# Kernel optimization log

Hardware: AMD Instinct MI355X
Metric: run time of the kernel (lower is better)

## Reference

```python
import jax, jax.numpy as jnp
import numpy as np

ALPHA = 1.702  # sigmoid-GLU scale
LIMIT = 7.0    # clamp limit
TOP_K = 2      # num_experts_per_tok


def setup_inputs() -> dict:
    key = jax.random.key(0)
    ks = jax.random.split(key, 4)
    B, S, H, E, I = 2, 1024, 1024, 8, 2048
    return {
        "hidden_states": jax.random.normal(ks[0], (B, S, H), jnp.float32),
        "router_weight": jax.random.normal(ks[1], (E, H), jnp.float32),
        "router_bias": jnp.zeros((E,), jnp.float32),
        "gate_up_proj": jax.random.normal(ks[2], (E, H, 2 * I), jnp.float32) * 0.02,
        "gate_up_bias": jnp.zeros((E, 2 * I), jnp.float32),
        "down_proj": jax.random.normal(ks[3], (E, I, H), jnp.float32) * 0.02,
        "down_bias": jnp.zeros((E, H), jnp.float32),
    }


def reference(hidden_states, router_weight, router_bias, gate_up_proj,
              gate_up_bias, down_proj, down_bias):
    B, S, H = hidden_states.shape
    E, _, two_I = gate_up_proj.shape
    I = two_I // 2

    flat = hidden_states.reshape(B * S, H)  # [T, H]

    # Router: softmax + top-k
    logits = flat @ router_weight.T + router_bias            # [T, E]
    scores = jax.nn.softmax(logits, axis=-1)
    topk_w, topk_idx = jax.lax.top_k(scores, TOP_K)          # [T, K]

    # Dense per-expert gated FFN (einsum 'abmh,ehn->abemn' computes all experts
    # on all tokens; the reshape/permute dance is a mathematical no-op).
    gu = jnp.einsum('th,ehn->ten', flat, gate_up_proj) + gate_up_bias  # [T, E, 2I]
    gate = jnp.minimum(gu[..., :I], LIMIT)
    up = jnp.clip(gu[..., I:], -LIMIT, LIMIT)
    glu = gate * jax.nn.sigmoid(gate * ALPHA)
    act = (up + 1.0) * glu                                   # [T, E, I]

    down = jnp.einsum('tei,eih->teh', act, down_proj) + down_bias  # [T, E, H]

    # Combine: gather each token's top-k expert outputs, weighted sum.
    gathered = jnp.take_along_axis(down, topk_idx[:, :, None], axis=1)  # [T, K, H]
    out = (gathered * topk_w[:, :, None]).sum(axis=1)        # [T, H]
    return out.reshape(B, S, H)
```

## Files before the change

kernel.cpp:

```cpp
#include <hip/hip_runtime.h>
#include <math.h>

#define TT 2048
#define HH 1024
#define EE 8
#define II 2048
#define N1 4096
#define ALPHA 1.702f
#define LIMIT 7.0f

typedef __attribute__((ext_vector_type(8))) short short8;
typedef __attribute__((ext_vector_type(4))) float floatx4;
typedef __attribute__((ext_vector_type(4))) unsigned int uintx4;

__device__ __forceinline__ short f2bf(float f) {
  union { float f; unsigned u; } v; v.f = f;
  unsigned r = (v.u + 0x7fffu + ((v.u >> 16) & 1u)) >> 16;
  return (short)r;
}
__device__ __forceinline__ unsigned cvt2(float lo, float hi) {
  unsigned r;
  asm("v_cvt_pk_bf16_f32 %0, %1, %2" : "=v"(r) : "v"(lo), "v"(hi));
  return r;
}
__device__ __forceinline__ void gload16(const void* g, void* l) {
  __builtin_amdgcn_global_load_lds(
      (const __attribute__((address_space(1))) unsigned int*)g,
      (__attribute__((address_space(3))) unsigned int*)l, 16, 0, 0);
}

__global__ __launch_bounds__(256) void transpose_all(
    const float* __restrict__ gup, const float* __restrict__ dp,
    unsigned short* __restrict__ gupt, unsigned short* __restrict__ dpt,
    int* __restrict__ counts) {
  const int id = blockIdx.x;
  if (id == 0 && threadIdx.x < 16) counts[threadIdx.x] = 0;
  const float* src;
  unsigned short* dst;
  int K, N, n0, k0, e;
  if (id < 8192) {
    src = gup; dst = gupt; K = HH; N = N1;
    n0 = (id & 63) * 64; k0 = ((id >> 6) & 15) * 64; e = id >> 10;
  } else {
    const int id2 = id - 8192;
    src = dp; dst = dpt; K = II; N = HH;
    n0 = (id2 & 15) * 64; k0 = ((id2 >> 4) & 31) * 64; e = id2 >> 9;
  }
  __shared__ float tile[64][68];
  const float* s = src + (size_t)e * K * N;
  unsigned short* d = dst + (size_t)e * N * K;
  const int t = threadIdx.x;
  const int nq = t & 15, kr = t >> 4;
#pragma unroll
  for (int r = 0; r < 4; r++) {
    const int k = r * 16 + kr;
    const float4 v = *(const float4*)(s + (size_t)(k0 + k) * N + n0 + nq * 4);
    tile[k][nq * 4 + 0] = v.x; tile[k][nq * 4 + 1] = v.y;
    tile[k][nq * 4 + 2] = v.z; tile[k][nq * 4 + 3] = v.w;
  }
  __syncthreads();
  const int n = t >> 2, ks = (t & 3) * 16;
  unsigned short* orow = d + (size_t)(n0 + n) * K + k0 + ks;
  uintx4 w0, w1;
#pragma unroll
  for (int m = 0; m < 4; m++)
    w0[m] = cvt2(tile[ks + 2 * m][n], tile[ks + 2 * m + 1][n]);
#pragma unroll
  for (int m = 0; m < 4; m++)
    w1[m] = cvt2(tile[ks + 8 + 2 * m][n], tile[ks + 9 + 2 * m][n]);
  *(uintx4*)orow = w0;
  *(uintx4*)(orow + 8) = w1;
}

__global__ __launch_bounds__(256) void router_kernel(
    const float* __restrict__ x, const float* __restrict__ rw,
    const float* __restrict__ rb, float* __restrict__ topk_w,
    int* __restrict__ counts, int* __restrict__ rows,
    unsigned short* __restrict__ xb, float* __restrict__ out) {
  const int t = blockIdx.x;
  const float* xr = x + (size_t)t * HH;
  const int lane = threadIdx.x & 63;
  const int wave = threadIdx.x >> 6;
  const float4 z = {0.f, 0.f, 0.f, 0.f};
  ((float4*)(out + (size_t)t * HH))[threadIdx.x] = z;
  float xv[16];
#pragma unroll
  for (int i = 0; i < 16; i++) xv[i] = xr[lane + i * 64];
  __shared__ float logits[EE];
#pragma unroll
  for (int ee = 0; ee < 2; ee++) {
    const int e = wave * 2 + ee;
    const float* wr = rw + (size_t)e * HH;
    float s = 0.f;
#pragma unroll
    for (int i = 0; i < 16; i++) s += xv[i] * wr[lane + i * 64];
#pragma unroll
    for (int off = 32; off > 0; off >>= 1) s += __shfl_down(s, off, 64);
    if (lane == 0) logits[e] = s + rb[e];
  }
  if (wave == 0) {
    unsigned short* xo = xb + (size_t)t * HH;
#pragma unroll
    for (int i = 0; i < 16; i++) xo[lane + i * 64] = (unsigned short)f2bf(xv[i]);
  }
  __syncthreads();
  if (threadIdx.x == 0) {
    float l[EE], sc[EE];
    float mx = -3.4e38f;
    for (int i = 0; i < EE; i++) { l[i] = logits[i]; mx = fmaxf(mx, l[i]); }
    float sum = 0.f;
    for (int i = 0; i < EE; i++) { sc[i] = expf(l[i] - mx); sum += sc[i]; }
    const float inv = 1.f / sum;
    int i0 = 0;
    for (int i = 1; i < EE; i++) if (sc[i] > sc[i0]) i0 = i;
    int i1 = (i0 == 0) ? 1 : 0;
    for (int i = 0; i < EE; i++) if (i != i0 && sc[i] > sc[i1]) i1 = i;
    topk_w[t * 2 + 0] = sc[i0] * inv;
    topk_w[t * 2 + 1] = sc[i1] * inv;
    const int s0 = atomicAdd(&counts[i0], 1);
    rows[i0 * TT + s0] = t * 2 + 0;
    const int s1 = atomicAdd(&counts[i1], 1);
    rows[i1 * TT + s1] = t * 2 + 1;
  }
}

__global__ __launch_bounds__(256, 4) void gemm_gu(
    const unsigned short* __restrict__ xb, const unsigned short* __restrict__ gupt,
    const float* __restrict__ gub, const int* __restrict__ counts,
    const int* __restrict__ rows, unsigned short* __restrict__ act) {
  const int swz = (blockIdx.x & 7) * (4096 / 8) + (blockIdx.x >> 3);
  const int mtile = swz & 15;
  const int ntile = (swz >> 4) & 31;
  const int e = swz >> 9;
  const int count = counts[e];
  if (mtile * 128 >= count) return;
  const int* rl = rows + e * TT + mtile * 128;
  __shared__ __align__(16) char smem[33280];
  unsigned short* As = (unsigned short*)smem;
  unsigned short* Bs = (unsigned short*)(smem + 16384);
  float* glds = (float*)smem;
  const int tid = threadIdx.x;
  const int lane = tid & 63, wave = tid >> 6;
  const int wm = (wave & 1) << 6, wn = (wave >> 1) << 6;
  const int quad = lane >> 4, r16 = lane & 15;

  const int lrow = lane >> 2, lko = (lane & 3) * 8;
  const int q0 = wave * 2, q1 = q0 + 1;
  const int row0 = q0 * 16 + lrow, row1 = q1 * 16 + lrow;
  const int last = count - 1 - mtile * 128;
  const int cr0 = row0 <= last ? row0 : last;
  const int cr1 = row1 <= last ? row1 : last;
  const unsigned short* pA0 = xb + (size_t)(rl[cr0] >> 1) * HH + lko;
  const unsigned short* pA1 = xb + (size_t)(rl[cr1] >> 1) * HH + lko;
  const int bn0 = (row0 < 64) ? (ntile * 64 + row0) : (II + ntile * 64 + row0 - 64);
  const int bn1 = (row1 < 64) ? (ntile * 64 + row1) : (II + ntile * 64 + row1 - 64);
  const unsigned short* pB0 = gupt + (size_t)e * N1 * HH + (size_t)bn0 * HH + lko;
  const unsigned short* pB1 = gupt + (size_t)e * N1 * HH + (size_t)bn1 * HH + lko;
  unsigned short* dA0 = As + q0 * 512;
  unsigned short* dA1 = As + q1 * 512;
  unsigned short* dB0 = Bs + q0 * 512;
  unsigned short* dB1 = Bs + q1 * 512;

  floatx4 acc[4][4] = {};
  const int NTK = HH / 32;

#define STAGE(B, kk) do { \
    const int ko_ = (kk) * 32; \
    gload16(pA0 + ko_, dA0 + (B) * 4096); \
    gload16(pA1 + ko_, dA1 + (B) * 4096); \
    gload16(pB0 + ko_, dB0 + (B) * 4096); \
    gload16(pB1 + ko_, dB1 + (B) * 4096); \
  } while (0)

#define PHASE(B) do { \
    asm volatile("s_waitcnt vmcnt(4)" ::: "memory"); \
    __builtin_amdgcn_s_barrier(); \
    short8 af[4], bf4[4]; \
    _Pragma("unroll") for (int i = 0; i < 4; i++) \
      af[i] = *(const short8*)(As + (B) * 4096 + (wm + i * 16 + r16) * 32 + quad * 8); \
    _Pragma("unroll") for (int j = 0; j < 4; j++) \
      bf4[j] = *(const short8*)(Bs + (B) * 4096 + (wn + j * 16 + r16) * 32 + quad * 8); \
    asm volatile("s_waitcnt lgkmcnt(0)" ::: "memory"); \
    __builtin_amdgcn_sched_barrier(0); \
    __builtin_amdgcn_s_barrier(); \
    { const int ks_ = kn < NTK ? kn : NTK - 1; kn++; STAGE(B, ks_); } \
    __builtin_amdgcn_sched_barrier(0); \
    __builtin_amdgcn_s_setprio(1); \
    _Pragma("unroll") for (int i = 0; i < 4; i++) \
      _Pragma("unroll") for (int j = 0; j < 4; j++) \
        acc[i][j] = __builtin_amdgcn_mfma_f32_16x16x32_bf16(af[i], bf4[j], acc[i][j], 0, 0, 0); \
    __builtin_amdgcn_s_setprio(0); \
  } while (0)

  STAGE(0, 0);
  STAGE(1, 1);
  int kn = 2;
#pragma unroll 1
  for (int t = 0; t < NTK; t += 2) {
    PHASE(0);
    PHASE(1);
  }
  asm volatile("s_waitcnt vmcnt(0)" ::: "memory");
  __builtin_amdgcn_s_barrier();

  const int colbase = ntile * 64;
  if (wn == 0) {
#pragma unroll
    for (int j = 0; j < 4; j++) {
      const int c = j * 16 + r16;
      const float gb = gub[e * N1 + colbase + c];
#pragma unroll
      for (int i = 0; i < 4; i++)
#pragma unroll
        for (int reg = 0; reg < 4; reg++) {
          const int rr = wm + i * 16 + quad * 4 + reg;
          float g = acc[i][j][reg] + gb;
          g = fminf(g, LIMIT);
          glds[rr * 65 + c] = g / (1.f + expf(-g * ALPHA));
        }
    }
  }
  __builtin_amdgcn_s_barrier();
  if (wn == 64) {
#pragma unroll
    for (int j = 0; j < 4; j++) {
      const int c = j * 16 + r16;
      const float ub = gub[e * N1 + II + colbase + c];
#pragma unroll
      for (int i = 0; i < 4; i++)
#pragma unroll
        for (int reg = 0; reg < 4; reg++) {
          const int rr = wm + i * 16 + quad * 4 + reg;
          if (mtile * 128 + rr < count) {
            float u = acc[i][j][reg] + ub;
            u = fminf(fmaxf(u, -LIMIT), LIMIT);
            const float glu = glds[rr * 65 + c];
            act[(size_t)rl[rr] * II + colbase + c] = (unsigned short)f2bf((u + 1.f) * glu);
          }
        }
    }
  }
#undef STAGE
#undef PHASE
}

__global__ __launch_bounds__(256, 4) void gemm_down(
    const unsigned short* __restrict__ act, const unsigned short* __restrict__ dpt,
    const float* __restrict__ db, const int* __restrict__ counts,
    const int* __restrict__ rows, const float* __restrict__ tw,
    float* __restrict__ out) {
  const int swz = (blockIdx.x & 7) * (2048 / 8) + (blockIdx.x >> 3);
  const int mtile = swz & 15;
  const int ntile = (swz >> 4) & 7;
  const int e = swz >> 8, kc = (swz >> 7) & 1;
  const int count = counts[e];
  if (mtile * 128 >= count) return;
  const int kb = kc * (II / 2);
  const int* rl = rows + e * TT + mtile * 128;
  __shared__ __align__(16) char smem[32768];
  unsigned short* As = (unsigned short*)smem;
  unsigned short* Bs = (unsigned short*)(smem + 16384);
  const int tid = threadIdx.x;
  const int lane = tid & 63, wave = tid >> 6;
  const int wm = (wave & 1) << 6, wn = (wave >> 1) << 6;
  const int quad = lane >> 4, r16 = lane & 15;

  const int lrow = lane >> 2, lko = (lane & 3) * 8;
  const int q0 = wave * 2, q1 = q0 + 1;
  const int row0 = q0 * 16 + lrow, row1 = q1 * 16 + lrow;
  const int last = count - 1 - mtile * 128;
  const int cr0 = row0 <= last ? row0 : last;
  const int cr1 = row1 <= last ? row1 : last;
  const unsigned short* pA0 = act + (size_t)rl[cr0] * II + kb + lko;
  const unsigned short* pA1 = act + (size_t)rl[cr1] * II + kb + lko;
  const unsigned short* pB0 = dpt + (size_t)e * HH * II + (size_t)(ntile * 128 + row0) * II + kb + lko;
  const unsigned short* pB1 = dpt + (size_t)e * HH * II + (size_t)(ntile * 128 + row1) * II + kb + lko;
  unsigned short* dA0 = As + q0 * 512;
  unsigned short* dA1 = As + q1 * 512;
  unsigned short* dB0 = Bs + q0 * 512;
  unsigned short* dB1 = Bs + q1 * 512;

  floatx4 acc[4][4] = {};
  const int NTK = (II / 2) / 32;

#define STAGE(B, kk) do { \
    const int ko_ = (kk) * 32; \
    gload16(pA0 + ko_, dA0 + (B) * 4096); \
    gload16(pA1 + ko_, dA1 + (B) * 4096); \
    gload16(pB0 + ko_, dB0 + (B) * 4096); \
    gload16(pB1 + ko_, dB1 + (B) * 4096); \
  } while (0)

#define PHASE(B) do { \
    asm volatile("s_waitcnt vmcnt(4)" ::: "memory"); \
    __builtin_amdgcn_s_barrier(); \
    short8 af[4], bf4[4]; \
    _Pragma("unroll") for (int i = 0; i < 4; i++) \
      af[i] = *(const short8*)(As + (B) * 4096 + (wm + i * 16 + r16) * 32 + quad * 8); \
    _Pragma("unroll") for (int j = 0; j < 4; j++) \
      bf4[j] = *(const short8*)(Bs + (B) * 4096 + (wn + j * 16 + r16) * 32 + quad * 8); \
    asm volatile("s_waitcnt lgkmcnt(0)" ::: "memory"); \
    __builtin_amdgcn_sched_barrier(0); \
    __builtin_amdgcn_s_barrier(); \
    { const int ks_ = kn < NTK ? kn : NTK - 1; kn++; STAGE(B, ks_); } \
    __builtin_amdgcn_sched_barrier(0); \
    __builtin_amdgcn_s_setprio(1); \
    _Pragma("unroll") for (int i = 0; i < 4; i++) \
      _Pragma("unroll") for (int j = 0; j < 4; j++) \
        acc[i][j] = __builtin_amdgcn_mfma_f32_16x16x32_bf16(af[i], bf4[j], acc[i][j], 0, 0, 0); \
    __builtin_amdgcn_s_setprio(0); \
  } while (0)

  STAGE(0, 0);
  STAGE(1, 1);
  int kn = 2;
#pragma unroll 1
  for (int t = 0; t < NTK; t += 2) {
    PHASE(0);
    PHASE(1);
  }
  asm volatile("s_waitcnt vmcnt(0)" ::: "memory");
  __builtin_amdgcn_s_barrier();

#pragma unroll
  for (int i = 0; i < 4; i++) {
#pragma unroll
    for (int reg = 0; reg < 4; reg++) {
      const int rr = wm + i * 16 + quad * 4 + reg;
      if (mtile * 128 + rr < count) {
        const int ent = rl[rr];
        const float w = tw[ent];
        float* orow = out + (size_t)(ent >> 1) * HH + ntile * 128;
#pragma unroll
        for (int j = 0; j < 4; j++) {
          const int c = wn + j * 16 + r16;
          float v = acc[i][j][reg];
          if (kc == 0) v += db[e * HH + ntile * 128 + c];
          atomicAdd(&orow[c], w * v);
        }
      }
    }
  }
#undef STAGE
#undef PHASE
}

extern "C" void kernel_launch(void* const* d_in, const int* in_sizes, int n_in,
                              void* d_out, int out_size, void* d_ws, size_t ws_size,
                              hipStream_t stream) {
  const float* x   = (const float*)d_in[0];
  const float* rw  = (const float*)d_in[1];
  const float* rb  = (const float*)d_in[2];
  const float* gup = (const float*)d_in[3];
  const float* gub = (const float*)d_in[4];
  const float* dp  = (const float*)d_in[5];
  const float* db  = (const float*)d_in[6];
  float* out = (float*)d_out;

  char* ws = (char*)d_ws;
  float* topk_w   = (float*)(ws + 0);
  int*   counts   = (int*)(ws + 16384);
  int*   rows     = (int*)(ws + 16640);
  unsigned short* xb   = (unsigned short*)(ws + 131072);
  unsigned short* gupt = (unsigned short*)(ws + 4325376);
  unsigned short* dpt  = (unsigned short*)(ws + 71434240);
  unsigned short* act  = (unsigned short*)(ws + 104988672);

  transpose_all<<<12288, 256, 0, stream>>>(gup, dp, gupt, dpt, counts);
  router_kernel<<<TT, 256, 0, stream>>>(x, rw, rb, topk_w, counts, rows, xb, out);
  gemm_gu<<<4096, 256, 0, stream>>>(xb, gupt, gub, counts, rows, act);
  gemm_down<<<2048, 256, 0, stream>>>(act, dpt, db, counts, rows, topk_w, out);
}
```

Measured before the change: 477.1 us.

## Use 256-row tiles with 512-thread blocks and fuse gate/up epilogue in registers

Both expert GEMMs move from 128x128 tiles on 256 threads to 256-row tiles on 512 threads (8 waves), so each weight tile is reused across twice as many routed tokens. The gate/up kernel interleaves gate and up columns so each wave holds matching gate and up accumulators, which removes the LDS round-trip and extra barrier in the GLU epilogue. The down GEMM splits K four ways instead of two, which adds more atomic adds to the output. The swizzled 1D grid becomes a plain 3D grid, which may change L2 locality, and the larger shared memory per block may lower occupancy.

```diff
diff --git a/kernel.cpp b/kernel.cpp
--- a/kernel.cpp
+++ b/kernel.cpp
@@ -124,60 +124,158 @@
   }
 }
 
-__global__ __launch_bounds__(256, 4) void gemm_gu(
+__global__ __launch_bounds__(512, 4) void gemm_gu(
     const unsigned short* __restrict__ xb, const unsigned short* __restrict__ gupt,
     const float* __restrict__ gub, const int* __restrict__ counts,
     const int* __restrict__ rows, unsigned short* __restrict__ act) {
-  const int swz = (blockIdx.x & 7) * (4096 / 8) + (blockIdx.x >> 3);
-  const int mtile = swz & 15;
-  const int ntile = (swz >> 4) & 31;
-  const int e = swz >> 9;
+  const int ntile = blockIdx.x, mtile = blockIdx.y, e = blockIdx.z;
   const int count = counts[e];
-  if (mtile * 128 >= count) return;
-  const int* rl = rows + e * TT + mtile * 128;
-  __shared__ __align__(16) char smem[33280];
+  if (mtile * 256 >= count) return;
+  const int* rl = rows + e * TT + mtile * 256;
+  __shared__ __align__(16) char smem[49152];
   unsigned short* As = (unsigned short*)smem;
-  unsigned short* Bs = (unsigned short*)(smem + 16384);
-  float* glds = (float*)smem;
+  unsigned short* Bs = (unsigned short*)(smem + 32768);
   const int tid = threadIdx.x;
   const int lane = tid & 63, wave = tid >> 6;
-  const int wm = (wave & 1) << 6, wn = (wave >> 1) << 6;
+  const int wm = (wave & 3) << 6;
+  const int wn = (wave >> 2) << 5;
   const int quad = lane >> 4, r16 = lane & 15;
-
   const int lrow = lane >> 2, lko = (lane & 3) * 8;
-  const int q0 = wave * 2, q1 = q0 + 1;
-  const int row0 = q0 * 16 + lrow, row1 = q1 * 16 + lrow;
-  const int last = count - 1 - mtile * 128;
-  const int cr0 = row0 <= last ? row0 : last;
-  const int cr1 = row1 <= last ? row1 : last;
+
+  const int ar0 = wave * 32 + lrow, ar1 = ar0 + 16;
+  const int last = count - 1 - mtile * 256;
+  const int cr0 = ar0 <= last ? ar0 : last;
+  const int cr1 = ar1 <= last ? ar1 : last;
   const unsigned short* pA0 = xb + (size_t)(rl[cr0] >> 1) * HH + lko;
   const unsigned short* pA1 = xb + (size_t)(rl[cr1] >> 1) * HH + lko;
-  const int bn0 = (row0 < 64) ? (ntile * 64 + row0) : (II + ntile * 64 + row0 - 64);
-  const int bn1 = (row1 < 64) ? (ntile * 64 + row1) : (II + ntile * 64 + row1 - 64);
-  const unsigned short* pB0 = gupt + (size_t)e * N1 * HH + (size_t)bn0 * HH + lko;
-  const unsigned short* pB1 = gupt + (size_t)e * N1 * HH + (size_t)bn1 * HH + lko;
-  unsigned short* dA0 = As + q0 * 512;
-  unsigned short* dA1 = As + q1 * 512;
-  unsigned short* dB0 = Bs + q0 * 512;
-  unsigned short* dB1 = Bs + q1 * 512;
+  const int br = wave * 16 + lrow;
+  const int bn = ntile * 64 + ((br >> 6) & 1) * 32 + (br & 31) + ((br >> 5) & 1) * II;
+  const unsigned short* pB = gupt + (size_t)e * N1 * HH + (size_t)bn * HH + lko;
+  unsigned short* dA0 = As + wave * 1024;
+  unsigned short* dA1 = dA0 + 512;
+  unsigned short* dB = Bs + wave * 512;
+
+  const int colw0 = wn + r16, colw1 = wn + 16 + r16;
+  const int grow0 = ((colw0 >> 5) << 6) + (colw0 & 31);
+  const int grow1 = ((colw1 >> 5) << 6) + (colw1 & 31);
 
   floatx4 acc[4][4] = {};
   const int NTK = HH / 32;
 
 #define STAGE(B, kk) do { \
     const int ko_ = (kk) * 32; \
-    gload16(pA0 + ko_, dA0 + (B) * 4096); \
-    gload16(pA1 + ko_, dA1 + (B) * 4096); \
-    gload16(pB0 + ko_, dB0 + (B) * 4096); \
-    gload16(pB1 + ko_, dB1 + (B) * 4096); \
+    gload16(pA0 + ko_, dA0 + (B) * 8192); \
+    gload16(pA1 + ko_, dA1 + (B) * 8192); \
+    gload16(pB + ko_, dB + (B) * 4096); \
   } while (0)
 
 #define PHASE(B) do { \
-    asm volatile("s_waitcnt vmcnt(4)" ::: "memory"); \
+    asm volatile("s_waitcnt vmcnt(3)" ::: "memory"); \
     __builtin_amdgcn_s_barrier(); \
     short8 af[4], bf4[4]; \
     _Pragma("unroll") for (int i = 0; i < 4; i++) \
-      af[i] = *(const short8*)(As + (B) * 4096 + (wm + i * 16 + r16) * 32 + quad * 8); \
+      af[i] = *(const short8*)(As + (B) * 8192 + (wm + i * 16 + r16) * 32 + quad * 8); \
+    bf4[0] = *(const short8*)(Bs + (B) * 4096 + grow0 * 32 + quad * 8); \
+    bf4[1] = *(const short8*)(Bs + (B) * 4096 + grow1 * 32 + quad * 8); \
+    bf4[2] = *(const short8*)(Bs + (B) * 4096 + (grow0 + 32) * 32 + quad * 8); \
+    bf4[3] = *(const short8*)(Bs + (B) * 4096 + (grow1 + 32) * 32 + quad * 8); \
+    asm volatile("s_waitcnt lgkmcnt(0)" ::: "memory"); \
+    __builtin_amdgcn_sched_barrier(0); \
+    __builtin_amdgcn_s_barrier(); \
+    { const int ks_ = kn < NTK ? kn : NTK - 1; kn++; STAGE(B, ks_); } \
+    __builtin_amdgcn_sched_barrier(0); \
+    __builtin_amdgcn_s_setprio(1); \
+    _Pragma("unroll") for (int i = 0; i < 4; i++) \
+      _Pragma("unroll") for (int j = 0; j < 4; j++) \
+        acc[i][j] = __builtin_amdgcn_mfma_f32_16x16x32_bf16(af[i], bf4[j], acc[i][j], 0, 0, 0); \
+    __builtin_amdgcn_s_setprio(0); \
+  } while (0)
+
+  STAGE(0, 0);
+  STAGE(1, 1);
+  int kn = 2;
+#pragma unroll 1
+  for (int t = 0; t < NTK; t += 2) {
+    PHASE(0);
+    PHASE(1);
+  }
+  asm volatile("s_waitcnt vmcnt(0)" ::: "memory");
+  __builtin_amdgcn_s_barrier();
+
+#pragma unroll
+  for (int j = 0; j < 2; j++) {
+    const int c = ntile * 64 + wn + j * 16 + r16;
+    const float gb = gub[e * N1 + c];
+    const float ub = gub[e * N1 + II + c];
+#pragma unroll
+    for (int i = 0; i < 4; i++) {
+#pragma unroll
+      for (int reg = 0; reg < 4; reg++) {
+        const int rr = wm + i * 16 + quad * 4 + reg;
+        if (mtile * 256 + rr < count) {
+          float g = acc[i][j][reg] + gb;
+          float u = acc[i][j + 2][reg] + ub;
+          g = fminf(g, LIMIT);
+          u = fminf(fmaxf(u, -LIMIT), LIMIT);
+          const float glu = g / (1.f + expf(-g * ALPHA));
+          act[(size_t)rl[rr] * II + c] = (unsigned short)f2bf((u + 1.f) * glu);
+        }
+      }
+    }
+  }
+#undef STAGE
+#undef PHASE
+}
+
+__global__ __launch_bounds__(512, 4) void gemm_down(
+    const unsigned short* __restrict__ act, const unsigned short* __restrict__ dpt,
+    const float* __restrict__ db, const int* __restrict__ counts,
+    const int* __restrict__ rows, const float* __restrict__ tw,
+    float* __restrict__ out) {
+  const int ntile = blockIdx.x, mtile = blockIdx.y;
+  const int e = blockIdx.z >> 2, kc = blockIdx.z & 3;
+  const int count = counts[e];
+  if (mtile * 256 >= count) return;
+  const int kb = kc * (II / 4);
+  const int* rl = rows + e * TT + mtile * 256;
+  __shared__ __align__(16) char smem[49152];
+  unsigned short* As = (unsigned short*)smem;
+  unsigned short* Bs = (unsigned short*)(smem + 32768);
+  const int tid = threadIdx.x;
+  const int lane = tid & 63, wave = tid >> 6;
+  const int wm = (wave & 3) << 6;
+  const int wn = (wave >> 2) << 6;
+  const int quad = lane >> 4, r16 = lane & 15;
+  const int lrow = lane >> 2, lko = (lane & 3) * 8;
+
+  const int ar0 = wave * 32 + lrow, ar1 = ar0 + 16;
+  const int last = count - 1 - mtile * 256;
+  const int cr0 = ar0 <= last ? ar0 : last;
+  const int cr1 = ar1 <= last ? ar1 : last;
+  const unsigned short* pA0 = act + (size_t)rl[cr0] * II + kb + lko;
+  const unsigned short* pA1 = act + (size_t)rl[cr1] * II + kb + lko;
+  const int br = wave * 16 + lrow;
+  const unsigned short* pB = dpt + (size_t)e * HH * II + (size_t)(ntile * 128 + br) * II + kb + lko;
+  unsigned short* dA0 = As + wave * 1024;
+  unsigned short* dA1 = dA0 + 512;
+  unsigned short* dB = Bs + wave * 512;
+
+  floatx4 acc[4][4] = {};
+  const int NTK = (II / 4) / 32;
+
+#define STAGE(B, kk) do { \
+    const int ko_ = (kk) * 32; \
+    gload16(pA0 + ko_, dA0 + (B) * 8192); \
+    gload16(pA1 + ko_, dA1 + (B) * 8192); \
+    gload16(pB + ko_, dB + (B) * 4096); \
+  } while (0)
+
+#define PHASE(B) do { \
+    asm volatile("s_waitcnt vmcnt(3)" ::: "memory"); \
+    __builtin_amdgcn_s_barrier(); \
+    short8 af[4], bf4[4]; \
+    _Pragma("unroll") for (int i = 0; i < 4; i++) \
+      af[i] = *(const short8*)(As + (B) * 8192 + (wm + i * 16 + r16) * 32 + quad * 8); \
     _Pragma("unroll") for (int j = 0; j < 4; j++) \
       bf4[j] = *(const short8*)(Bs + (B) * 4096 + (wn + j * 16 + r16) * 32 + quad * 8); \
     asm volatile("s_waitcnt lgkmcnt(0)" ::: "memory"); \
@@ -203,131 +301,12 @@
   asm volatile("s_waitcnt vmcnt(0)" ::: "memory");
   __builtin_amdgcn_s_barrier();
 
-  const int colbase = ntile * 64;
-  if (wn == 0) {
-#pragma unroll
-    for (int j = 0; j < 4; j++) {
-      const int c = j * 16 + r16;
-      const float gb = gub[e * N1 + colbase + c];
-#pragma unroll
-      for (int i = 0; i < 4; i++)
-#pragma unroll
-        for (int reg = 0; reg < 4; reg++) {
-          const int rr = wm + i * 16 + quad * 4 + reg;
-          float g = acc[i][j][reg] + gb;
-          g = fminf(g, LIMIT);
-          glds[rr * 65 + c] = g / (1.f + expf(-g * ALPHA));
-        }
-    }
-  }
-  __builtin_amdgcn_s_barrier();
-  if (wn == 64) {
-#pragma unroll
-    for (int j = 0; j < 4; j++) {
-      const int c = j * 16 + r16;
-      const float ub = gub[e * N1 + II + colbase + c];
-#pragma unroll
-      for (int i = 0; i < 4; i++)
-#pragma unroll
-        for (int reg = 0; reg < 4; reg++) {
-          const int rr = wm + i * 16 + quad * 4 + reg;
-          if (mtile * 128 + rr < count) {
-            float u = acc[i][j][reg] + ub;
-            u = fminf(fmaxf(u, -LIMIT), LIMIT);
-            const float glu = glds[rr * 65 + c];
-            act[(size_t)rl[rr] * II + colbase + c] = (unsigned short)f2bf((u + 1.f) * glu);
-          }
-        }
-    }
-  }
-#undef STAGE
-#undef PHASE
-}
-
-__global__ __launch_bounds__(256, 4) void gemm_down(
-    const unsigned short* __restrict__ act, const unsigned short* __restrict__ dpt,
-    const float* __restrict__ db, const int* __restrict__ counts,
-    const int* __restrict__ rows, const float* __restrict__ tw,
-    float* __restrict__ out) {
-  const int swz = (blockIdx.x & 7) * (2048 / 8) + (blockIdx.x >> 3);
-  const int mtile = swz & 15;
-  const int ntile = (swz >> 4) & 7;
-  const int e = swz >> 8, kc = (swz >> 7) & 1;
-  const int count = counts[e];
-  if (mtile * 128 >= count) return;
-  const int kb = kc * (II / 2);
-  const int* rl = rows + e * TT + mtile * 128;
-  __shared__ __align__(16) char smem[32768];
-  unsigned short* As = (unsigned short*)smem;
-  unsigned short* Bs = (unsigned short*)(smem + 16384);
-  const int tid = threadIdx.x;
-  const int lane = tid & 63, wave = tid >> 6;
-  const int wm = (wave & 1) << 6, wn = (wave >> 1) << 6;
-  const int quad = lane >> 4, r16 = lane & 15;
-
-  const int lrow = lane >> 2, lko = (lane & 3) * 8;
-  const int q0 = wave * 2, q1 = q0 + 1;
-  const int row0 = q0 * 16 + lrow, row1 = q1 * 16 + lrow;
-  const int last = count - 1 - mtile * 128;
-  const int cr0 = row0 <= last ? row0 : last;
-  const int cr1 = row1 <= last ? row1 : last;
-  const unsigned short* pA0 = act + (size_t)rl[cr0] * II + kb + lko;
-  const unsigned short* pA1 = act + (size_t)rl[cr1] * II + kb + lko;
-  const unsigned short* pB0 = dpt + (size_t)e * HH * II + (size_t)(ntile * 128 + row0) * II + kb + lko;
-  const unsigned short* pB1 = dpt + (size_t)e * HH * II + (size_t)(ntile * 128 + row1) * II + kb + lko;
-  unsigned short* dA0 = As + q0 * 512;
-  unsigned short* dA1 = As + q1 * 512;
-  unsigned short* dB0 = Bs + q0 * 512;
-  unsigned short* dB1 = Bs + q1 * 512;
-
-  floatx4 acc[4][4] = {};
-  const int NTK = (II / 2) / 32;
-
-#define STAGE(B, kk) do { \
-    const int ko_ = (kk) * 32; \
-    gload16(pA0 + ko_, dA0 + (B) * 4096); \
-    gload16(pA1 + ko_, dA1 + (B) * 4096); \
-    gload16(pB0 + ko_, dB0 + (B) * 4096); \
-    gload16(pB1 + ko_, dB1 + (B) * 4096); \
-  } while (0)
-
-#define PHASE(B) do { \
-    asm volatile("s_waitcnt vmcnt(4)" ::: "memory"); \
-    __builtin_amdgcn_s_barrier(); \
-    short8 af[4], bf4[4]; \
-    _Pragma("unroll") for (int i = 0; i < 4; i++) \
-      af[i] = *(const short8*)(As + (B) * 4096 + (wm + i * 16 + r16) * 32 + quad * 8); \
-    _Pragma("unroll") for (int j = 0; j < 4; j++) \
-      bf4[j] = *(const short8*)(Bs + (B) * 4096 + (wn + j * 16 + r16) * 32 + quad * 8); \
-    asm volatile("s_waitcnt lgkmcnt(0)" ::: "memory"); \
-    __builtin_amdgcn_sched_barrier(0); \
-    __builtin_amdgcn_s_barrier(); \
-    { const int ks_ = kn < NTK ? kn : NTK - 1; kn++; STAGE(B, ks_); } \
-    __builtin_amdgcn_sched_barrier(0); \
-    __builtin_amdgcn_s_setprio(1); \
-    _Pragma("unroll") for (int i = 0; i < 4; i++) \
-      _Pragma("unroll") for (int j = 0; j < 4; j++) \
-        acc[i][j] = __builtin_amdgcn_mfma_f32_16x16x32_bf16(af[i], bf4[j], acc[i][j], 0, 0, 0); \
-    __builtin_amdgcn_s_setprio(0); \
-  } while (0)
-
-  STAGE(0, 0);
-  STAGE(1, 1);
-  int kn = 2;
-#pragma unroll 1
-  for (int t = 0; t < NTK; t += 2) {
-    PHASE(0);
-    PHASE(1);
-  }
-  asm volatile("s_waitcnt vmcnt(0)" ::: "memory");
-  __builtin_amdgcn_s_barrier();
-
 #pragma unroll
   for (int i = 0; i < 4; i++) {
 #pragma unroll
     for (int reg = 0; reg < 4; reg++) {
       const int rr = wm + i * 16 + quad * 4 + reg;
-      if (mtile * 128 + rr < count) {
+      if (mtile * 256 + rr < count) {
         const int ent = rl[rr];
         const float w = tw[ent];
         float* orow = out + (size_t)(ent >> 1) * HH + ntile * 128;
@@ -368,6 +347,6 @@
 
   transpose_all<<<12288, 256, 0, stream>>>(gup, dp, gupt, dpt, counts);
   router_kernel<<<TT, 256, 0, stream>>>(x, rw, rb, topk_w, counts, rows, xb, out);
-  gemm_gu<<<4096, 256, 0, stream>>>(xb, gupt, gub, counts, rows, act);
-  gemm_down<<<2048, 256, 0, stream>>>(act, dpt, db, counts, rows, topk_w, out);
-}
+  gemm_gu<<<dim3(II / 64, 8, EE), 512, 0, stream>>>(xb, gupt, gub, counts, rows, act);
+  gemm_down<<<dim3(HH / 128, 8, EE * 4), 512, 0, stream>>>(act, dpt, db, counts, rows, topk_w, out);
+}
```

Result: no change. 477.9 us (+0.2%).
